# Performance work log

Measured on AMD Instinct MI355X. Metric: run time of the kernel, lower is better.

The kernel has to match this reference:

```python
import jax, jax.numpy as jnp
import numpy as np

N, D, IN, HID, OUT, E = 20000, 8, 64, 128, 64, 100000
EPS = 1e-5


def _bn(h, g, b):
    # training-mode BatchNorm1d: biased batch variance, eps=1e-5
    m = h.mean(axis=0)
    v = jnp.mean((h - m) ** 2, axis=0)
    return (h - m) * jax.lax.rsqrt(v + EPS) * g + b


def setup_inputs() -> dict:
    key = jax.random.key(0)
    ks = jax.random.split(key, 12)
    x = jax.random.normal(ks[0], (N, IN), dtype=jnp.float32)
    node_ts = jax.random.uniform(ks[1], (N,), dtype=jnp.float32)
    neighbor_idx = jax.random.randint(ks[2], (N, D), 0, N, dtype=jnp.int32)
    neighbor_ts = jax.random.uniform(ks[3], (N, D), dtype=jnp.float32)
    target = jax.random.randint(ks[4], (2, E), 0, N, dtype=jnp.int32)
    neg_pairs = jax.random.randint(ks[5], (2, E), 0, N, dtype=jnp.int32)
    W1 = jax.random.normal(ks[6], (IN, HID), dtype=jnp.float32) * (1.0 / np.sqrt(IN))
    b1 = jnp.zeros((HID,), jnp.float32)
    g1 = jnp.ones((HID,), jnp.float32)
    be1 = jnp.zeros((HID,), jnp.float32)
    W2 = jax.random.normal(ks[7], (HID, OUT), dtype=jnp.float32) * (1.0 / np.sqrt(HID))
    b2 = jnp.zeros((OUT,), jnp.float32)
    g2 = jnp.ones((OUT,), jnp.float32)
    be2 = jnp.zeros((OUT,), jnp.float32)
    Wd = jax.random.normal(ks[8], (OUT, 1), dtype=jnp.float32) * (1.0 / np.sqrt(OUT))
    bd = jnp.zeros((1,), jnp.float32)
    return {"x": x, "node_ts": node_ts, "neighbor_idx": neighbor_idx,
            "neighbor_ts": neighbor_ts, "target": target, "neg_pairs": neg_pairs,
            "W1": W1, "b1": b1, "g1": g1, "be1": be1,
            "W2": W2, "b2": b2, "g2": g2, "be2": be2, "Wd": Wd, "bd": bd}


def reference(x, node_ts, neighbor_idx, neighbor_ts, target, neg_pairs,
              W1, b1, g1, be1, W2, b2, g2, be2, Wd, bd):
    n = jnp.arange(N, dtype=neighbor_idx.dtype)
    # ---- level-2 queries: every node at its own timestamp ----
    # children = D temporal-neighbor slots + self (self always valid, ts=node_ts)
    c_idx = jnp.concatenate([neighbor_idx, n[:, None]], axis=1)          # [N, D+1]
    c_ts = jnp.concatenate([neighbor_ts, node_ts[:, None]], axis=1)      # [N, D+1]
    mask2 = jnp.concatenate([neighbor_ts <= node_ts[:, None],
                             jnp.ones((N, 1), bool)], axis=1)            # [N, D+1]
    # ---- level-1 queries: each (child node, child ts) pair ----
    ci = c_idx.reshape(-1)                                               # [M]
    cts = c_ts.reshape(-1)
    gc_idx = jnp.concatenate([neighbor_idx[ci], ci[:, None]], axis=1)    # [M, D+1]
    mask1 = jnp.concatenate([neighbor_ts[ci] <= cts[:, None],
                             jnp.ones((ci.shape[0], 1), bool)], axis=1)
    # ---- layer 0: raw features of grandchildren ----
    h0 = x[gc_idx]                                                       # [M, D+1, IN]
    m1 = mask1.astype(x.dtype)
    agg1 = jnp.einsum('mk,mkf->mf', m1, h0) / m1.sum(1, keepdims=True)   # masked mean
    h1 = jax.nn.relu(_bn(agg1 @ W1 + b1, g1, be1))                       # [M, HID]
    h1 = h1.reshape(N, D + 1, HID)
    # ---- layer 2 aggregation over temporal children ----
    m2 = mask2.astype(x.dtype)
    agg2 = jnp.einsum('nk,nkf->nf', m2, h1) / m2.sum(1, keepdims=True)
    embs = jax.nn.relu(_bn(agg2 @ W2 + b2, g2, be2))                     # [N, OUT]
    # ---- HadNet link decoder + BCEWithLogits ----
    pos = (embs[target[0]] * embs[target[1]]) @ Wd + bd                  # [E, 1]
    neg = (embs[neg_pairs[0]] * embs[neg_pairs[1]]) @ Wd + bd            # [E, 1]
    preds = jnp.concatenate([pos, neg], axis=0)[:, 0]                    # [2E]
    labels = jnp.concatenate([jnp.ones((E,), x.dtype), jnp.zeros((E,), x.dtype)])
    loss = jnp.mean(jnp.maximum(preds, 0.0) - preds * labels
                    + jnp.log1p(jnp.exp(-jnp.abs(preds))))
    return loss
```

## Files before the change

kernel.cpp:

```cpp
#include <hip/hip_runtime.h>
#include <math.h>

constexpr int kN = 20000;
constexpr int kD = 8;
constexpr int kE = 100000;
constexpr int kM = kN * 9;
constexpr int kTiles1 = kM / 16;
constexpr int kTilesN = kN / 16;
constexpr float kEps = 1e-5f;

constexpr int S_SUM1 = 0, S_SQ1 = 128, S_SUM2 = 256, S_SQ2 = 320;

constexpr size_t OFF_M     = 0;
constexpr size_t OFF_PRE2  = 23040000;
constexpr size_t OFF_STATS = 25600000;
constexpr size_t OFF_CNT   = 25601536;
constexpr size_t OFF_RI    = 26321536;

typedef short short8 __attribute__((ext_vector_type(8)));
typedef float floatx4 __attribute__((ext_vector_type(4)));

__device__ __forceinline__ unsigned f2bf(float f) {
  unsigned u = __float_as_uint(f);
  u += 0x7fffu + ((u >> 16) & 1u);
  return u >> 16;
}

__global__ __launch_bounds__(256) void k0_prefix(
    const float* __restrict__ x, const float* __restrict__ node_ts,
    const int* __restrict__ nidx, const float* __restrict__ nts,
    unsigned short* __restrict__ M, int* __restrict__ rowinfo,
    float* __restrict__ cntf, float* __restrict__ out)
{
  if (blockIdx.x == 0 && threadIdx.x == 0) *out = 0.f;

  int c = blockIdx.x * 4 + (threadIdx.x >> 6);
  const int lane = threadIdx.x & 63;
  c = __builtin_amdgcn_readfirstlane(c);

  float ts[8]; int id[8];
#pragma unroll
  for (int j = 0; j < kD; ++j) { ts[j] = nts[c * kD + j]; id[j] = nidx[c * kD + j]; }

#define CSWAP(A, B)                                                   \
  { float ta = ts[A], tb = ts[B]; int ia = id[A], ib = id[B];         \
    bool sw = tb < ta;                                                \
    ts[A] = sw ? tb : ta; ts[B] = sw ? ta : tb;                       \
    id[A] = sw ? ib : ia; id[B] = sw ? ia : ib; }
  CSWAP(0, 1) CSWAP(2, 3) CSWAP(0, 2) CSWAP(1, 3) CSWAP(1, 2)
  CSWAP(4, 5) CSWAP(6, 7) CSWAP(4, 6) CSWAP(5, 7) CSWAP(5, 6)
  CSWAP(0, 4) CSWAP(1, 5) CSWAP(2, 6) CSWAP(3, 7)
  CSWAP(2, 4) CSWAP(3, 5)
  CSWAP(1, 2) CSWAP(3, 4) CSWAP(5, 6)
#undef CSWAP

  float s = x[c * 64 + lane];
  unsigned short* mp = M + (size_t)c * 9 * 64 + lane;
  mp[0] = (unsigned short)f2bf(s);
#pragma unroll
  for (int r = 1; r <= kD; ++r) {
    s += x[id[r - 1] * 64 + lane];
    mp[r * 64] = (unsigned short)f2bf(s / (float)(r + 1));
  }

  const int m = blockIdx.x * 256 + threadIdx.x;
  if (m < kM) {
    const int n = (int)((unsigned)m / 9u);
    const int slot = m - n * 9;
    int cc; float t;
    if (slot < kD) { cc = nidx[n * kD + slot]; t = nts[n * kD + slot]; }
    else           { cc = n;                   t = node_ts[n]; }
    int rank = 0;
#pragma unroll
    for (int j = 0; j < kD; ++j) rank += (nts[cc * kD + j] <= t) ? 1 : 0;
    rowinfo[m] = cc * 9 + rank;
    atomicAdd(&cntf[cc * 9 + rank], 1.0f);
  }
}

__global__ __launch_bounds__(256, 3) void k1_stats(
    const unsigned short* __restrict__ M, const float* __restrict__ cntf,
    const float* __restrict__ W1, const float* __restrict__ b1,
    float* __restrict__ stats)
{
  __shared__ unsigned short W1T[128 * 72];
  __shared__ float redS[256][8];
  __shared__ float redQ[256][8];

  const int tid = threadIdx.x;
  const int lane = tid & 63;
  const int wave = tid >> 6;
  const int l15 = lane & 15;
  const int q = lane >> 4;

  for (int i = tid; i < 8192; i += 256) {
    int n = i >> 6, k = i & 63;
    W1T[n * 72 + k] = (unsigned short)f2bf(W1[k * 128 + n]);
  }
  __syncthreads();

  short8 bf[8][2];
#pragma unroll
  for (int cc = 0; cc < 8; ++cc)
#pragma unroll
    for (int s = 0; s < 2; ++s)
      bf[cc][s] = *(const short8*)&W1T[(cc * 16 + l15) * 72 + q * 8 + s * 32];

  float b1c[8];
#pragma unroll
  for (int cc = 0; cc < 8; ++cc) b1c[cc] = b1[cc * 16 + l15];

  float sum8[8], sq8[8];
#pragma unroll
  for (int cc = 0; cc < 8; ++cc) { sum8[cc] = 0.f; sq8[cc] = 0.f; }

  const int gw = blockIdx.x * 4 + wave;
  const int nw = gridDim.x * 4;

  for (int t = gw; t < kTiles1; t += nw) {
    const unsigned short* mp = M + (size_t)(t * 16 + l15) * 64;
    short8 af0 = *(const short8*)(mp + q * 8);
    short8 af1 = *(const short8*)(mp + 32 + q * 8);
    float c4[4];
#pragma unroll
    for (int i = 0; i < 4; ++i) c4[i] = cntf[t * 16 + q * 4 + i];

    floatx4 acc[8];
#pragma unroll
    for (int cc = 0; cc < 8; ++cc) {
      acc[cc] = (floatx4){0.f, 0.f, 0.f, 0.f};
      acc[cc] = __builtin_amdgcn_mfma_f32_16x16x32_bf16(af0, bf[cc][0], acc[cc], 0, 0, 0);
      acc[cc] = __builtin_amdgcn_mfma_f32_16x16x32_bf16(af1, bf[cc][1], acc[cc], 0, 0, 0);
    }
#pragma unroll
    for (int cc = 0; cc < 8; ++cc) {
#pragma unroll
      for (int i = 0; i < 4; ++i) {
        float v = acc[cc][i] + b1c[cc];
        sum8[cc] += c4[i] * v;
        sq8[cc]  += c4[i] * v * v;
      }
    }
  }

  __syncthreads();
#pragma unroll
  for (int cc = 0; cc < 8; ++cc) { redS[tid][cc] = sum8[cc]; redQ[tid][cc] = sq8[cc]; }
  __syncthreads();
  if (tid < 128) {
    int cc = tid >> 4, r15 = tid & 15;
    float s = 0.f, qq = 0.f;
#pragma unroll
    for (int w = 0; w < 4; ++w)
#pragma unroll
      for (int p = 0; p < 4; ++p) {
        int T = w * 64 + p * 16 + r15;
        s += redS[T][cc]; qq += redQ[T][cc];
      }
    atomicAdd(&stats[S_SUM1 + tid], s);
    atomicAdd(&stats[S_SQ1 + tid], qq);
  }
}

__global__ __launch_bounds__(256, 3) void k3_fused(
    const unsigned short* __restrict__ M, const int* __restrict__ rowinfo,
    const float* __restrict__ node_ts, const float* __restrict__ nts,
    const float* __restrict__ stats_in, const float* __restrict__ g1,
    const float* __restrict__ be1, const float* __restrict__ W1,
    const float* __restrict__ b1, const float* __restrict__ W2,
    const float* __restrict__ b2, float* __restrict__ stats_out,
    unsigned short* __restrict__ pre2)
{
  __shared__ __attribute__((aligned(16))) char lds[42496];
  unsigned short* W1T = (unsigned short*)lds;
  unsigned short* W2T = (unsigned short*)(lds + 18432);
  unsigned short* sm   = (unsigned short*)lds;
  unsigned short* aggT = (unsigned short*)(lds + 38016);
  float* winv = (float*)(lds + 42368);

  const int tid = threadIdx.x;
  const int lane = tid & 63;
  const int wave = tid >> 6;
  const int l15 = lane & 15;
  const int q = lane >> 4;

  for (int i = tid; i < 8192; i += 256) {
    int nn = i >> 6, k = i & 63;
    W1T[nn * 72 + k] = (unsigned short)f2bf(W1[k * 128 + nn]);
  }
  for (int i = tid; i < 8192; i += 256) {
    int nn = i >> 7, k = i & 127;
    W2T[nn * 136 + k] = (unsigned short)f2bf(W2[k * 64 + nn]);
  }
  __syncthreads();

  short8 bf[8][2];
  float scc[8], shc[8];
#pragma unroll
  for (int cc = 0; cc < 8; ++cc) {
    int col = cc * 16 + l15;
#pragma unroll
    for (int s = 0; s < 2; ++s)
      bf[cc][s] = *(const short8*)&W1T[col * 72 + q * 8 + s * 32];
    float mean = stats_in[S_SUM1 + col] * (1.f / kM);
    float var  = stats_in[S_SQ1 + col] * (1.f / kM) - mean * mean;
    float sg   = g1[col] * rsqrtf(var + kEps);
    scc[cc] = sg;
    shc[cc] = (b1[col] - mean) * sg + be1[col];
  }
  short8 bfr2[4];
#pragma unroll
  for (int s = 0; s < 4; ++s)
    bfr2[s] = *(const short8*)&W2T[(wave * 16 + l15) * 136 + q * 8 + s * 32];
  const float b2w = b2[wave * 16 + l15];
  __syncthreads();

  float sumS = 0.f, sumQ = 0.f;

  for (int tb = blockIdx.x; tb < kTilesN; tb += 625) {
    const int node0 = tb * 16;
    const int row0 = tb * 144;

    if (tid < 16) {
      int nn = node0 + tid;
      float tn = node_ts[nn];
      float sw = 1.f;
#pragma unroll
      for (int j = 0; j < kD; ++j) sw += (nts[nn * kD + j] <= tn) ? 1.f : 0.f;
      winv[tid] = 1.f / sw;
    }

    for (int tl = wave; tl < 9; tl += 4) {
      const int ri = rowinfo[row0 + tl * 16 + l15];
      const unsigned short* mp = M + (size_t)ri * 64;
      short8 af0 = *(const short8*)(mp + q * 8);
      short8 af1 = *(const short8*)(mp + 32 + q * 8);

      float w4[4];
#pragma unroll
      for (int i = 0; i < 4; ++i) {
        int gm = row0 + tl * 16 + q * 4 + i;
        int n = (int)((unsigned)gm / 9u);
        int slot = gm - n * 9;
        w4[i] = (slot < kD) ? ((nts[n * kD + slot] <= node_ts[n]) ? 1.f : 0.f)
                            : 1.f;
      }

      floatx4 acc[8];
#pragma unroll
      for (int cc = 0; cc < 8; ++cc) {
        acc[cc] = (floatx4){0.f, 0.f, 0.f, 0.f};
        acc[cc] = __builtin_amdgcn_mfma_f32_16x16x32_bf16(af0, bf[cc][0], acc[cc], 0, 0, 0);
        acc[cc] = __builtin_amdgcn_mfma_f32_16x16x32_bf16(af1, bf[cc][1], acc[cc], 0, 0, 0);
      }
#pragma unroll
      for (int cc = 0; cc < 8; ++cc) {
        int col = cc * 16 + l15;
#pragma unroll
        for (int i = 0; i < 4; ++i) {
          float val = fmaxf(fmaf(acc[cc][i], scc[cc], shc[cc]), 0.f) * w4[i];
          sm[(tl * 16 + q * 4 + i) * 132 + col] = (unsigned short)f2bf(val);
        }
      }
    }
    __syncthreads();

#pragma unroll
    for (int k = 0; k < 4; ++k) {
      int it = tid + k * 256;
      int nd = it >> 6, cp = it & 63;
      float s0 = 0.f, s1 = 0.f;
#pragma unroll
      for (int r = 0; r < 9; ++r) {
        unsigned u = *(const unsigned*)&sm[(nd * 9 + r) * 132 + cp * 2];
        s0 += __uint_as_float(u << 16);
        s1 += __uint_as_float(u & 0xffff0000u);
      }
      float iv = winv[nd];
      *(unsigned*)&aggT[nd * 136 + cp * 2] = f2bf(s0 * iv) | (f2bf(s1 * iv) << 16);
    }
    __syncthreads();

    short8 af2[4];
#pragma unroll
    for (int s = 0; s < 4; ++s)
      af2[s] = *(const short8*)&aggT[l15 * 136 + q * 8 + s * 32];
    floatx4 acc2 = (floatx4){0.f, 0.f, 0.f, 0.f};
#pragma unroll
    for (int s = 0; s < 4; ++s)
      acc2 = __builtin_amdgcn_mfma_f32_16x16x32_bf16(af2[s], bfr2[s], acc2, 0, 0, 0);
#pragma unroll
    for (int i = 0; i < 4; ++i) {
      float v = acc2[i] + b2w;
      int nrow = node0 + q * 4 + i;
      pre2[(size_t)nrow * 64 + wave * 16 + l15] = (unsigned short)f2bf(v);
      sumS += v; sumQ += v * v;
    }
  }

  sumS += __shfl_xor(sumS, 16); sumS += __shfl_xor(sumS, 32);
  sumQ += __shfl_xor(sumQ, 16); sumQ += __shfl_xor(sumQ, 32);
  if (lane < 16) {
    atomicAdd(&stats_out[S_SUM2 + wave * 16 + lane], sumS);
    atomicAdd(&stats_out[S_SQ2 + wave * 16 + lane], sumQ);
  }
}

__global__ __launch_bounds__(256) void k6_loss(
    const unsigned short* __restrict__ pre2, const float* __restrict__ stats,
    const float* __restrict__ g2, const float* __restrict__ be2,
    const float* __restrict__ Wd, const int* __restrict__ tgt,
    const int* __restrict__ neg, const float* __restrict__ bd,
    float* __restrict__ out)
{
  __shared__ float scl[64], shl[64], wdl[64];
  __shared__ float redl[256];
  const int tid = threadIdx.x;
  if (tid < 64) {
    float mean = stats[S_SUM2 + tid] * (1.f / kN);
    float var  = stats[S_SQ2 + tid] * (1.f / kN) - mean * mean;
    float s    = g2[tid] * rsqrtf(var + kEps);
    scl[tid] = s; shl[tid] = be2[tid] - mean * s; wdl[tid] = Wd[tid];
  }
  __syncthreads();

  const int tq = tid & 15;
  const int qb = tid >> 4;
  const int c0 = tq * 4;
  const float4 sc4 = {scl[c0], scl[c0 + 1], scl[c0 + 2], scl[c0 + 3]};
  const float4 sh4 = {shl[c0], shl[c0 + 1], shl[c0 + 2], shl[c0 + 3]};
  const float4 wd4 = {wdl[c0], wdl[c0 + 1], wdl[c0 + 2], wdl[c0 + 3]};
  const float bd0 = bd[0];

  float lsum = 0.f;
  const int e0 = blockIdx.x * 128 + qb * 8;
#pragma unroll
  for (int it = 0; it < 8; ++it) {
    int e = e0 + it;
    if (e < 2 * kE) {
      int i, j; float lab;
      if (e < kE) { i = tgt[e];      j = tgt[kE + e]; lab = 1.f; }
      else        { i = neg[e - kE]; j = neg[e];      lab = 0.f; }
      uint2 ua = *(const uint2*)&pre2[(size_t)i * 64 + c0];
      uint2 ub = *(const uint2*)&pre2[(size_t)j * 64 + c0];
      float a0 = __uint_as_float(ua.x << 16), a1 = __uint_as_float(ua.x & 0xffff0000u);
      float a2 = __uint_as_float(ua.y << 16), a3 = __uint_as_float(ua.y & 0xffff0000u);
      float b0 = __uint_as_float(ub.x << 16), b1v = __uint_as_float(ub.x & 0xffff0000u);
      float b2v = __uint_as_float(ub.y << 16), b3 = __uint_as_float(ub.y & 0xffff0000u);
      float ei0 = fmaxf(fmaf(a0, sc4.x, sh4.x), 0.f) * wd4.x;
      float ei1 = fmaxf(fmaf(a1, sc4.y, sh4.y), 0.f) * wd4.y;
      float ei2 = fmaxf(fmaf(a2, sc4.z, sh4.z), 0.f) * wd4.z;
      float ei3 = fmaxf(fmaf(a3, sc4.w, sh4.w), 0.f) * wd4.w;
      float ej0 = fmaxf(fmaf(b0, sc4.x, sh4.x), 0.f);
      float ej1 = fmaxf(fmaf(b1v, sc4.y, sh4.y), 0.f);
      float ej2 = fmaxf(fmaf(b2v, sc4.z, sh4.z), 0.f);
      float ej3 = fmaxf(fmaf(b3, sc4.w, sh4.w), 0.f);
      float p = ei0 * ej0 + ei1 * ej1 + ei2 * ej2 + ei3 * ej3;
      p += __shfl_xor(p, 1); p += __shfl_xor(p, 2);
      p += __shfl_xor(p, 4); p += __shfl_xor(p, 8);
      p += bd0;
      float l = fmaxf(p, 0.f) - p * lab + log1pf(expf(-fabsf(p)));
      if (tq == 0) lsum += l;
    }
  }
  redl[tid] = lsum;
  __syncthreads();
  for (int s = 128; s > 0; s >>= 1) {
    if (tid < s) redl[tid] += redl[tid + s];
    __syncthreads();
  }
  if (tid == 0) atomicAdd(out, redl[0] * (1.f / (2 * kE)));
}

extern "C" void kernel_launch(void* const* d_in, const int* in_sizes, int n_in,
                              void* d_out, int out_size, void* d_ws, size_t ws_size,
                              hipStream_t stream) {
  (void)in_sizes; (void)n_in; (void)out_size; (void)ws_size;
  const float* x       = (const float*)d_in[0];
  const float* node_ts = (const float*)d_in[1];
  const int*   nidx    = (const int*)d_in[2];
  const float* nts     = (const float*)d_in[3];
  const int*   tgt     = (const int*)d_in[4];
  const int*   neg     = (const int*)d_in[5];
  const float* W1      = (const float*)d_in[6];
  const float* b1      = (const float*)d_in[7];
  const float* g1      = (const float*)d_in[8];
  const float* be1     = (const float*)d_in[9];
  const float* W2      = (const float*)d_in[10];
  const float* b2      = (const float*)d_in[11];
  const float* g2      = (const float*)d_in[12];
  const float* be2     = (const float*)d_in[13];
  const float* Wd      = (const float*)d_in[14];
  const float* bd      = (const float*)d_in[15];

  char* ws = (char*)d_ws;
  unsigned short* Mbuf = (unsigned short*)(ws + OFF_M);
  unsigned short* pre2 = (unsigned short*)(ws + OFF_PRE2);
  float* stats = (float*)(ws + OFF_STATS);
  float* cntf  = (float*)(ws + OFF_CNT);
  int*   rinfo = (int*)(ws + OFF_RI);
  float* out   = (float*)d_out;

  hipMemsetAsync(ws + OFF_STATS, 0, 1536 + 720000, stream);

  k0_prefix<<<kN / 4, 256, 0, stream>>>(x, node_ts, nidx, nts, Mbuf, rinfo,
                                        cntf, out);
  k1_stats<<<704, 256, 0, stream>>>(Mbuf, cntf, W1, b1, stats);
  k3_fused<<<625, 256, 0, stream>>>(Mbuf, rinfo, node_ts, nts, stats, g1, be1,
                                    W1, b1, W2, b2, stats, pre2);
  k6_loss<<<(2 * kE + 127) / 128, 256, 0, stream>>>(pre2, stats, g2, be2, Wd,
                                                    tgt, neg, bd, out);
}
```

Measured before the change: 214.4 us.

## Prefetch row indices across tiles and un-alias LDS buffers in fused GEMM kernel

The fused layer-1/layer-2 kernel now prefetches the next tile's row indices in registers and issues all A-fragment loads up front. The masked weights are computed once per tile into LDS instead of being recomputed per lane with divides. Weight and staging buffers get separate LDS arrays, which removes the aliasing and one barrier. The grid shrinks from 625 to 512 persistent blocks and launch bounds drop to 2 blocks per SM. This trades more LDS use and lower occupancy for latency hiding, and 512 blocks over 1250 tiles gives an uneven tail.

```diff
diff --git a/kernel.cpp b/kernel.cpp
--- a/kernel.cpp
+++ b/kernel.cpp
@@ -162,7 +162,7 @@
   }
 }
 
-__global__ __launch_bounds__(256, 3) void k3_fused(
+__global__ __launch_bounds__(256, 2) void k3_fused(
     const unsigned short* __restrict__ M, const int* __restrict__ rowinfo,
     const float* __restrict__ node_ts, const float* __restrict__ nts,
     const float* __restrict__ stats_in, const float* __restrict__ g1,
@@ -171,18 +171,24 @@
     const float* __restrict__ b2, float* __restrict__ stats_out,
     unsigned short* __restrict__ pre2)
 {
-  __shared__ __attribute__((aligned(16))) char lds[42496];
-  unsigned short* W1T = (unsigned short*)lds;
-  unsigned short* W2T = (unsigned short*)(lds + 18432);
-  unsigned short* sm   = (unsigned short*)lds;
-  unsigned short* aggT = (unsigned short*)(lds + 38016);
-  float* winv = (float*)(lds + 42368);
+  __shared__ __attribute__((aligned(16))) unsigned short W1T[128 * 72];
+  __shared__ __attribute__((aligned(16))) unsigned short W2T[64 * 136];
+  __shared__ __attribute__((aligned(16))) unsigned short sm[144 * 132];
+  __shared__ __attribute__((aligned(16))) unsigned short aggT[16 * 136];
+  __shared__ float wlds[144];
+  __shared__ float winv[16];
 
   const int tid = threadIdx.x;
   const int lane = tid & 63;
   const int wave = tid >> 6;
   const int l15 = lane & 15;
   const int q = lane >> 4;
+
+  int tb = blockIdx.x;
+  int ri0 = rowinfo[tb * 144 + wave * 16 + l15];
+  int ri1 = rowinfo[tb * 144 + 64 + wave * 16 + l15];
+  int ri2 = 0;
+  if (wave == 0) ri2 = rowinfo[tb * 144 + 128 + l15];
 
   for (int i = tid; i < 8192; i += 256) {
     int nn = i >> 6, k = i & 63;
@@ -213,56 +219,76 @@
   for (int s = 0; s < 4; ++s)
     bfr2[s] = *(const short8*)&W2T[(wave * 16 + l15) * 136 + q * 8 + s * 32];
   const float b2w = b2[wave * 16 + l15];
-  __syncthreads();
 
   float sumS = 0.f, sumQ = 0.f;
 
-  for (int tb = blockIdx.x; tb < kTilesN; tb += 625) {
+  for (; tb < kTilesN; tb += gridDim.x) {
     const int node0 = tb * 16;
-    const int row0 = tb * 144;
-
+
+    const unsigned short* mp0 = M + (size_t)ri0 * 64;
+    const unsigned short* mp1 = M + (size_t)ri1 * 64;
+    short8 a00 = *(const short8*)(mp0 + q * 8);
+    short8 a01 = *(const short8*)(mp0 + 32 + q * 8);
+    short8 a10 = *(const short8*)(mp1 + q * 8);
+    short8 a11 = *(const short8*)(mp1 + 32 + q * 8);
+    short8 a20{}, a21{};
+    if (wave == 0) {
+      const unsigned short* mp2 = M + (size_t)ri2 * 64;
+      a20 = *(const short8*)(mp2 + q * 8);
+      a21 = *(const short8*)(mp2 + 32 + q * 8);
+    }
+
+    {
+      int ntb = tb + gridDim.x;
+      if (ntb < kTilesN) {
+        ri0 = rowinfo[ntb * 144 + wave * 16 + l15];
+        ri1 = rowinfo[ntb * 144 + 64 + wave * 16 + l15];
+        if (wave == 0) ri2 = rowinfo[ntb * 144 + 128 + l15];
+      }
+    }
+
+    if (tid < 144) {
+      int ln = tid / 9;
+      int slot = tid - ln * 9;
+      int nn = node0 + ln;
+      float w = 1.f;
+      if (slot < kD) w = (nts[nn * kD + slot] <= node_ts[nn]) ? 1.f : 0.f;
+      wlds[tid] = w;
+    }
+    __syncthreads();
     if (tid < 16) {
-      int nn = node0 + tid;
-      float tn = node_ts[nn];
-      float sw = 1.f;
-#pragma unroll
-      for (int j = 0; j < kD; ++j) sw += (nts[nn * kD + j] <= tn) ? 1.f : 0.f;
-      winv[tid] = 1.f / sw;
-    }
-
-    for (int tl = wave; tl < 9; tl += 4) {
-      const int ri = rowinfo[row0 + tl * 16 + l15];
-      const unsigned short* mp = M + (size_t)ri * 64;
-      short8 af0 = *(const short8*)(mp + q * 8);
-      short8 af1 = *(const short8*)(mp + 32 + q * 8);
-
-      float w4[4];
-#pragma unroll
-      for (int i = 0; i < 4; ++i) {
-        int gm = row0 + tl * 16 + q * 4 + i;
-        int n = (int)((unsigned)gm / 9u);
-        int slot = gm - n * 9;
-        w4[i] = (slot < kD) ? ((nts[n * kD + slot] <= node_ts[n]) ? 1.f : 0.f)
-                            : 1.f;
-      }
-
-      floatx4 acc[8];
-#pragma unroll
-      for (int cc = 0; cc < 8; ++cc) {
-        acc[cc] = (floatx4){0.f, 0.f, 0.f, 0.f};
-        acc[cc] = __builtin_amdgcn_mfma_f32_16x16x32_bf16(af0, bf[cc][0], acc[cc], 0, 0, 0);
-        acc[cc] = __builtin_amdgcn_mfma_f32_16x16x32_bf16(af1, bf[cc][1], acc[cc], 0, 0, 0);
-      }
-#pragma unroll
-      for (int cc = 0; cc < 8; ++cc) {
-        int col = cc * 16 + l15;
-#pragma unroll
-        for (int i = 0; i < 4; ++i) {
-          float val = fmaxf(fmaf(acc[cc][i], scc[cc], shc[cc]), 0.f) * w4[i];
-          sm[(tl * 16 + q * 4 + i) * 132 + col] = (unsigned short)f2bf(val);
-        }
-      }
-    }
+      float swv = 0.f;
+#pragma unroll
+      for (int r = 0; r < 9; ++r) swv += wlds[tid * 9 + r];
+      winv[tid] = 1.f / swv;
+    }
+
+#define ROWTILE(TL, A0, A1)                                                  \
+    {                                                                        \
+      floatx4 acc[8];                                                        \
+      _Pragma("unroll")                                                      \
+      for (int cc = 0; cc < 8; ++cc) {                                       \
+        acc[cc] = (floatx4){0.f, 0.f, 0.f, 0.f};                             \
+        acc[cc] = __builtin_amdgcn_mfma_f32_16x16x32_bf16(A0, bf[cc][0], acc[cc], 0, 0, 0); \
+        acc[cc] = __builtin_amdgcn_mfma_f32_16x16x32_bf16(A1, bf[cc][1], acc[cc], 0, 0, 0); \
+      }                                                                      \
+      float w4[4];                                                           \
+      _Pragma("unroll")                                                      \
+      for (int i = 0; i < 4; ++i) w4[i] = wlds[(TL) * 16 + q * 4 + i];       \
+      _Pragma("unroll")                                                      \
+      for (int cc = 0; cc < 8; ++cc) {                                       \
+        int col = cc * 16 + l15;                                             \
+        _Pragma("unroll")                                                    \
+        for (int i = 0; i < 4; ++i) {                                        \
+          float val = fmaxf(fmaf(acc[cc][i], scc[cc], shc[cc]), 0.f) * w4[i];\
+          sm[((TL) * 16 + q * 4 + i) * 132 + col] = (unsigned short)f2bf(val);\
+        }                                                                    \
+      }                                                                      \
+    }
+    ROWTILE(wave, a00, a01)
+    ROWTILE(wave + 4, a10, a11)
+    if (wave == 0) ROWTILE(8, a20, a21)
+#undef ROWTILE
     __syncthreads();
 
 #pragma unroll
@@ -406,7 +432,7 @@
   k0_prefix<<<kN / 4, 256, 0, stream>>>(x, node_ts, nidx, nts, Mbuf, rinfo,
                                         cntf, out);
   k1_stats<<<704, 256, 0, stream>>>(Mbuf, cntf, W1, b1, stats);
-  k3_fused<<<625, 256, 0, stream>>>(Mbuf, rinfo, node_ts, nts, stats, g1, be1,
+  k3_fused<<<512, 256, 0, stream>>>(Mbuf, rinfo, node_ts, nts, stats, g1, be1,
                                     W1, b1, W2, b2, stats, pre2);
   k6_loss<<<(2 * kE + 127) / 128, 256, 0, stream>>>(pre2, stats, g2, be2, Wd,
                                                     tgt, neg, bd, out);
```

Measured after the change: 201.7 us. 5.9% less time.

## Aggregate per-node MFMA rows in registers and double-buffer agg tile

Applied to the files above, without the earlier changes.

The layer-1 matmul tiles are realigned so that each 16-row MFMA tile covers the 9 children of one node, padded to 16 rows. The masked mean is then done in registers with shuffles, which removes the large bf16 staging buffer in shared memory, one sync and the LDS reduction pass. A double-buffered aggT tile removes the second barrier, and the next tile's rowinfo indices are prefetched. In exchange, 7 of every 16 MFMA rows are padding, so tensor-core work rises by about 16/9, and the grid stride now depends on gridDim.

```diff
diff --git a/kernel.cpp b/kernel.cpp
--- a/kernel.cpp
+++ b/kernel.cpp
@@ -171,18 +171,24 @@
     const float* __restrict__ b2, float* __restrict__ stats_out,
     unsigned short* __restrict__ pre2)
 {
-  __shared__ __attribute__((aligned(16))) char lds[42496];
+  __shared__ __attribute__((aligned(16))) char lds[35840];
   unsigned short* W1T = (unsigned short*)lds;
   unsigned short* W2T = (unsigned short*)(lds + 18432);
-  unsigned short* sm   = (unsigned short*)lds;
-  unsigned short* aggT = (unsigned short*)(lds + 38016);
-  float* winv = (float*)(lds + 42368);
+  unsigned short* aggT0 = (unsigned short*)lds;
+  unsigned short* aggT1 = (unsigned short*)(lds + 4352);
 
   const int tid = threadIdx.x;
   const int lane = tid & 63;
   const int wave = tid >> 6;
   const int l15 = lane & 15;
   const int q = lane >> 4;
+
+  int tb = blockIdx.x;
+  const int sl = (l15 < 9) ? l15 : 0;
+  int ri[4];
+#pragma unroll
+  for (int j = 0; j < 4; ++j)
+    ri[j] = rowinfo[(tb * 16 + wave * 4 + j) * 9 + sl];
 
   for (int i = tid; i < 8192; i += 256) {
     int nn = i >> 6, k = i & 63;
@@ -217,74 +223,77 @@
 
   float sumS = 0.f, sumQ = 0.f;
 
-  for (int tb = blockIdx.x; tb < kTilesN; tb += 625) {
+  int parity = 0;
+  for (; tb < kTilesN; tb += gridDim.x, parity ^= 1) {
     const int node0 = tb * 16;
-    const int row0 = tb * 144;
-
-    if (tid < 16) {
-      int nn = node0 + tid;
-      float tn = node_ts[nn];
-      float sw = 1.f;
-#pragma unroll
-      for (int j = 0; j < kD; ++j) sw += (nts[nn * kD + j] <= tn) ? 1.f : 0.f;
-      winv[tid] = 1.f / sw;
-    }
-
-    for (int tl = wave; tl < 9; tl += 4) {
-      const int ri = rowinfo[row0 + tl * 16 + l15];
-      const unsigned short* mp = M + (size_t)ri * 64;
-      short8 af0 = *(const short8*)(mp + q * 8);
-      short8 af1 = *(const short8*)(mp + 32 + q * 8);
-
+    unsigned short* aggW = parity ? aggT1 : aggT0;
+
+    short8 a0[4], a1[4];
+#pragma unroll
+    for (int j = 0; j < 4; ++j) {
+      const unsigned short* mp = M + (size_t)ri[j] * 64;
+      a0[j] = *(const short8*)(mp + q * 8);
+      a1[j] = *(const short8*)(mp + 32 + q * 8);
+    }
+
+    {
+      int ntb = tb + gridDim.x;
+      if (ntb < kTilesN) {
+#pragma unroll
+        for (int j = 0; j < 4; ++j)
+          ri[j] = rowinfo[(ntb * 16 + wave * 4 + j) * 9 + sl];
+      }
+    }
+
+#pragma unroll
+    for (int j = 0; j < 4; ++j) {
+      const int n = node0 + wave * 4 + j;
+      const float tn = node_ts[n];
+      float wsl[8], swv = 1.f;
+#pragma unroll
+      for (int s = 0; s < kD; ++s) {
+        wsl[s] = (nts[n * kD + s] <= tn) ? 1.f : 0.f;
+        swv += wsl[s];
+      }
+      const float iv = 1.f / swv;
       float w4[4];
 #pragma unroll
       for (int i = 0; i < 4; ++i) {
-        int gm = row0 + tl * 16 + q * 4 + i;
-        int n = (int)((unsigned)gm / 9u);
-        int slot = gm - n * 9;
-        w4[i] = (slot < kD) ? ((nts[n * kD + slot] <= node_ts[n]) ? 1.f : 0.f)
-                            : 1.f;
+        int slot = q * 4 + i;
+        w4[i] = (slot < 8) ? wsl[slot] : ((slot == 8) ? 1.f : 0.f);
       }
 
       floatx4 acc[8];
 #pragma unroll
       for (int cc = 0; cc < 8; ++cc) {
         acc[cc] = (floatx4){0.f, 0.f, 0.f, 0.f};
-        acc[cc] = __builtin_amdgcn_mfma_f32_16x16x32_bf16(af0, bf[cc][0], acc[cc], 0, 0, 0);
-        acc[cc] = __builtin_amdgcn_mfma_f32_16x16x32_bf16(af1, bf[cc][1], acc[cc], 0, 0, 0);
-      }
+        acc[cc] = __builtin_amdgcn_mfma_f32_16x16x32_bf16(a0[j], bf[cc][0], acc[cc], 0, 0, 0);
+        acc[cc] = __builtin_amdgcn_mfma_f32_16x16x32_bf16(a1[j], bf[cc][1], acc[cc], 0, 0, 0);
+      }
+      float p[8];
 #pragma unroll
       for (int cc = 0; cc < 8; ++cc) {
-        int col = cc * 16 + l15;
-#pragma unroll
-        for (int i = 0; i < 4; ++i) {
-          float val = fmaxf(fmaf(acc[cc][i], scc[cc], shc[cc]), 0.f) * w4[i];
-          sm[(tl * 16 + q * 4 + i) * 132 + col] = (unsigned short)f2bf(val);
-        }
+        float s = 0.f;
+#pragma unroll
+        for (int i = 0; i < 4; ++i)
+          s += fmaxf(fmaf(acc[cc][i], scc[cc], shc[cc]), 0.f) * w4[i];
+        s += __shfl_xor(s, 16);
+        s += __shfl_xor(s, 32);
+        p[cc] = s * iv;
+      }
+      if (q == 0) {
+        int r = (wave * 4 + j) * 136 + l15;
+#pragma unroll
+        for (int cc = 0; cc < 8; ++cc)
+          aggW[r + cc * 16] = (unsigned short)f2bf(p[cc]);
       }
     }
     __syncthreads();
 
-#pragma unroll
-    for (int k = 0; k < 4; ++k) {
-      int it = tid + k * 256;
-      int nd = it >> 6, cp = it & 63;
-      float s0 = 0.f, s1 = 0.f;
-#pragma unroll
-      for (int r = 0; r < 9; ++r) {
-        unsigned u = *(const unsigned*)&sm[(nd * 9 + r) * 132 + cp * 2];
-        s0 += __uint_as_float(u << 16);
-        s1 += __uint_as_float(u & 0xffff0000u);
-      }
-      float iv = winv[nd];
-      *(unsigned*)&aggT[nd * 136 + cp * 2] = f2bf(s0 * iv) | (f2bf(s1 * iv) << 16);
-    }
-    __syncthreads();
-
     short8 af2[4];
 #pragma unroll
     for (int s = 0; s < 4; ++s)
-      af2[s] = *(const short8*)&aggT[l15 * 136 + q * 8 + s * 32];
+      af2[s] = *(const short8*)&aggW[l15 * 136 + q * 8 + s * 32];
     floatx4 acc2 = (floatx4){0.f, 0.f, 0.f, 0.f};
 #pragma unroll
     for (int s = 0; s < 4; ++s)
```

Result: no change. 217.0 us (+1.2%).
